# Optimization experiments

Hardware: AMD Instinct MI355X
Metric: run time of the kernel (lower is better)

The kernel has to match this reference:

```python
import jax, jax.numpy as jnp
import numpy as np

N, C, H, W = 32, 1, 512, 1024
SAMPLE_NUM = 5000
SIGMA = 0.03
ALPHA = 1.0
EPS = 1e-6
LOSS_WEIGHT = 1.0


def setup_inputs() -> dict:
    key = jax.random.key(0)
    k0, k1, k2, k3 = jax.random.split(key, 4)
    prediction = jax.random.normal(k0, (N, C, H, W), dtype=jnp.float32)
    # depths strictly > 0 so target > mask_value (=-1e-8) holds for every pixel,
    # matching the common case where all pixels are 'effective'.
    target = jax.random.uniform(k1, (N, C, H, W), dtype=jnp.float32,
                                minval=0.1, maxval=10.0)
    mask = jax.random.randint(k2, (N, C, H, W), 0, 2).astype(bool)
    # per-image random permutation of pixel indices -> disjoint pairs (A, B),
    # reproducing torch.randperm-based pair sampling as constant indices.
    perm = jax.vmap(lambda k: jax.random.permutation(k, H * W))(
        jax.random.split(k3, N))                      # [N, H*W] int32
    idx_A = perm[:, 0:2 * SAMPLE_NUM:2]               # [N, S]
    idx_B = perm[:, 1:2 * SAMPLE_NUM:2]               # [N, S]
    return {"prediction": prediction, "target": target, "mask": mask,
            "idx_A": idx_A, "idx_B": idx_B}


def reference(prediction, target, mask, idx_A, idx_B):
    n = target.shape[0]
    p = prediction.reshape(n, -1)   # [N, H*W]
    t = target.reshape(n, -1)
    m = mask.reshape(n, -1)

    iA = jnp.take_along_axis(p, idx_A, axis=1)   # [N, S]
    iB = jnp.take_along_axis(p, idx_B, axis=1)
    tA = jnp.take_along_axis(t, idx_A, axis=1)
    tB = jnp.take_along_axis(t, idx_B, axis=1)
    mA = jnp.take_along_axis(m, idx_A, axis=1)
    mB = jnpp_take(m, idx_B) if False else jnp.take_along_axis(m, idx_B, axis=1)

    ratio = tA / (tB + EPS)
    hi = 1.0 + SIGMA
    lo = 1.0 / (1.0 + SIGMA)
    mask_eq = (ratio < hi) & (ratio > lo)
    labels = jnp.where(ratio >= hi, 1.0,
                       jnp.where(ratio <= lo, -1.0, 0.0)).astype(p.dtype)
    cmask = mA & mB

    eq_sel = mask_eq & cmask
    uneq_sel = (~mask_eq) & cmask

    equal_loss = jnp.where(eq_sel, (iA - iB) ** 2, 0.0).sum()
    unequal_loss = jnp.where(
        uneq_sel, jnp.log1p(jnp.exp((iB - iA) * labels)), 0.0).sum()
    valid_samples = cmask.sum().astype(p.dtype)

    loss = (ALPHA * equal_loss + unequal_loss) / (valid_samples + EPS)
    return loss * LOSS_WEIGHT
```

## Files before the change

kernel.cpp:

```cpp
#include <hip/hip_runtime.h>
#include <math.h>

#define SAMPLE_NUM 5000
#define HWSZ (512 * 1024)
#define SIGMA_F 0.03f
#define EPS_F 1e-6f

template <bool MASK_I32>
__device__ __forceinline__ void
process_pairs(const float* __restrict__ pred, const float* __restrict__ targ,
              const void* __restrict__ mask_raw, const int* __restrict__ idxA,
              const int* __restrict__ idxB, int total, float& eq_sum,
              float& uneq_sum, float& valid) {
  const float hi = 1.0f + SIGMA_F;
  const float lo = 1.0f / (1.0f + SIGMA_F);
  const int* m32 = (const int*)mask_raw;
  const unsigned char* m8 = (const unsigned char*)mask_raw;

  const int i = blockIdx.x * blockDim.x + threadIdx.x;
  if (i >= total) return;

  const int n = i / SAMPLE_NUM;
  const long long base = (long long)n * HWSZ;
  const int a = idxA[i];
  const int b = idxB[i];
  const long long ia_off = base + a;
  const long long ib_off = base + b;

  const int ma = MASK_I32 ? m32[ia_off] : (int)m8[ia_off];
  const int mb = MASK_I32 ? m32[ib_off] : (int)m8[ib_off];
  const float tA = targ[ia_off];
  const float tB = targ[ib_off];
  const float iA = pred[ia_off];
  const float iB = pred[ib_off];

  const bool cm = (ma != 0) && (mb != 0);
  const float ratio = tA / (tB + EPS_F);
  const bool is_eq = (ratio < hi) && (ratio > lo);
  const float d = iA - iB;
  const float label = (ratio >= hi) ? 1.0f : -1.0f;
  const float x = (iB - iA) * label;
  const float u = (x > 20.0f) ? x : log1pf(expf(x));

  eq_sum += (cm && is_eq) ? d * d : 0.0f;
  uneq_sum += (cm && !is_eq) ? u : 0.0f;
  valid += cm ? 1.0f : 0.0f;
}

__global__ void __launch_bounds__(256)
ranking_loss_kernel(const float* __restrict__ pred,
                    const float* __restrict__ targ,
                    const void* __restrict__ mask_raw,
                    const int* __restrict__ idxA,
                    const int* __restrict__ idxB,
                    float* __restrict__ out,
                    float* __restrict__ ws,
                    int total) {
  const unsigned int* mw = (const unsigned int*)mask_raw;
  bool mask_is_i32 = true;
  #pragma unroll
  for (int w = 0; w < 32; ++w) {
    if (mw[w] > 1u) mask_is_i32 = false;
  }

  float eq_sum = 0.0f, uneq_sum = 0.0f, valid = 0.0f;
  if (mask_is_i32) {
    process_pairs<true>(pred, targ, mask_raw, idxA, idxB, total, eq_sum,
                        uneq_sum, valid);
  } else {
    process_pairs<false>(pred, targ, mask_raw, idxA, idxB, total, eq_sum,
                         uneq_sum, valid);
  }

  #pragma unroll
  for (int off = 32; off > 0; off >>= 1) {
    eq_sum   += __shfl_down(eq_sum, off, 64);
    uneq_sum += __shfl_down(uneq_sum, off, 64);
    valid    += __shfl_down(valid, off, 64);
  }

  __shared__ float s_eq[4], s_un[4], s_va[4];
  const int lane = threadIdx.x & 63;
  const int wave = threadIdx.x >> 6;
  if (lane == 0) {
    s_eq[wave] = eq_sum;
    s_un[wave] = uneq_sum;
    s_va[wave] = valid;
  }
  __syncthreads();

  if (threadIdx.x == 0) {
    float e = 0.0f, u = 0.0f, v = 0.0f;
    const int nwaves = blockDim.x >> 6;
    for (int w = 0; w < nwaves; ++w) {
      e += s_eq[w];
      u += s_un[w];
      v += s_va[w];
    }
    atomicAdd(&ws[0], e);
    atomicAdd(&ws[1], u);
    atomicAdd(&ws[2], v);
    __threadfence();
    const unsigned int ticket = atomicAdd((unsigned int*)&ws[3], 1u);
    if (ticket == gridDim.x - 1) {
      const float eqs = atomicAdd(&ws[0], 0.0f);
      const float uns = atomicAdd(&ws[1], 0.0f);
      const float vas = atomicAdd(&ws[2], 0.0f);
      out[0] = (eqs + uns) / (vas + EPS_F);
    }
  }
}

extern "C" void kernel_launch(void* const* d_in, const int* in_sizes, int n_in,
                              void* d_out, int out_size, void* d_ws,
                              size_t ws_size, hipStream_t stream) {
  const float* pred = (const float*)d_in[0];
  const float* targ = (const float*)d_in[1];
  const void* mask = d_in[2];
  const int* idxA = (const int*)d_in[3];
  const int* idxB = (const int*)d_in[4];
  float* out = (float*)d_out;
  float* ws = (float*)d_ws;

  const int total = in_sizes[3];

  hipMemsetAsync(d_ws, 0, 4 * sizeof(float), stream);

  const int block = 256;
  const int grid = (total + block - 1) / block;
  ranking_loss_kernel<<<grid, block, 0, stream>>>(pred, targ, mask, idxA, idxB,
                                                  out, ws, total);
}
```

Measured before the change: 208.3 us.

## Replace atomic ticket reduction with per-block partials and finalize kernel; skip masked loads

Each block now writes its three partial sums to its own workspace slot, and a second single-block kernel reduces those slots and computes the loss. This removes the memset and the contended global float atomics and ticket counter, at the cost of one extra kernel launch. The per-pair body also loads target and prediction only when both mask bits are set, which skips gather traffic for masked pairs but adds divergent branches.

```diff
diff --git a/kernel.cpp b/kernel.cpp
--- a/kernel.cpp
+++ b/kernel.cpp
@@ -5,19 +5,21 @@
 #define HWSZ (512 * 1024)
 #define SIGMA_F 0.03f
 #define EPS_F 1e-6f
+#define BLOCK 256
+
 
 template <bool MASK_I32>
 __device__ __forceinline__ void
-process_pairs(const float* __restrict__ pred, const float* __restrict__ targ,
-              const void* __restrict__ mask_raw, const int* __restrict__ idxA,
-              const int* __restrict__ idxB, int total, float& eq_sum,
-              float& uneq_sum, float& valid) {
+pair_body(const float* __restrict__ pred, const float* __restrict__ targ,
+          const void* __restrict__ mask_raw, const int* __restrict__ idxA,
+          const int* __restrict__ idxB, int total, float& eq_sum,
+          float& uneq_sum, float& valid) {
   const float hi = 1.0f + SIGMA_F;
   const float lo = 1.0f / (1.0f + SIGMA_F);
   const int* m32 = (const int*)mask_raw;
   const unsigned char* m8 = (const unsigned char*)mask_raw;
 
-  const int i = blockIdx.x * blockDim.x + threadIdx.x;
+  const int i = blockIdx.x * BLOCK + threadIdx.x;
   if (i >= total) return;
 
   const int n = i / SAMPLE_NUM;
@@ -29,33 +31,33 @@
 
   const int ma = MASK_I32 ? m32[ia_off] : (int)m8[ia_off];
   const int mb = MASK_I32 ? m32[ib_off] : (int)m8[ib_off];
-  const float tA = targ[ia_off];
-  const float tB = targ[ib_off];
-  const float iA = pred[ia_off];
-  const float iB = pred[ib_off];
 
-  const bool cm = (ma != 0) && (mb != 0);
-  const float ratio = tA / (tB + EPS_F);
-  const bool is_eq = (ratio < hi) && (ratio > lo);
-  const float d = iA - iB;
-  const float label = (ratio >= hi) ? 1.0f : -1.0f;
-  const float x = (iB - iA) * label;
-  const float u = (x > 20.0f) ? x : log1pf(expf(x));
+  if (ma && mb) {
+    const float tA = targ[ia_off];
+    const float tB = targ[ib_off];
+    const float iA = pred[ia_off];
+    const float iB = pred[ib_off];
 
-  eq_sum += (cm && is_eq) ? d * d : 0.0f;
-  uneq_sum += (cm && !is_eq) ? u : 0.0f;
-  valid += cm ? 1.0f : 0.0f;
+    valid += 1.0f;
+    const float ratio = tA / (tB + EPS_F);
+    if (ratio < hi && ratio > lo) {
+      const float d = iA - iB;
+      eq_sum += d * d;
+    } else {
+      const float label = (ratio >= hi) ? 1.0f : -1.0f;
+      const float x = (iB - iA) * label;
+      uneq_sum += (x > 20.0f) ? x : log1pf(expf(x));
+    }
+  }
 }
 
-__global__ void __launch_bounds__(256)
-ranking_loss_kernel(const float* __restrict__ pred,
-                    const float* __restrict__ targ,
-                    const void* __restrict__ mask_raw,
-                    const int* __restrict__ idxA,
-                    const int* __restrict__ idxB,
-                    float* __restrict__ out,
-                    float* __restrict__ ws,
-                    int total) {
+__global__ void __launch_bounds__(BLOCK)
+ranking_loss_partial(const float* __restrict__ pred,
+                     const float* __restrict__ targ,
+                     const void* __restrict__ mask_raw,
+                     const int* __restrict__ idxA,
+                     const int* __restrict__ idxB,
+                     float* __restrict__ ws, int total) {
   const unsigned int* mw = (const unsigned int*)mask_raw;
   bool mask_is_i32 = true;
   #pragma unroll
@@ -65,11 +67,11 @@
 
   float eq_sum = 0.0f, uneq_sum = 0.0f, valid = 0.0f;
   if (mask_is_i32) {
-    process_pairs<true>(pred, targ, mask_raw, idxA, idxB, total, eq_sum,
-                        uneq_sum, valid);
+    pair_body<true>(pred, targ, mask_raw, idxA, idxB, total, eq_sum, uneq_sum,
+                    valid);
   } else {
-    process_pairs<false>(pred, targ, mask_raw, idxA, idxB, total, eq_sum,
-                         uneq_sum, valid);
+    pair_body<false>(pred, targ, mask_raw, idxA, idxB, total, eq_sum, uneq_sum,
+                     valid);
   }
 
   #pragma unroll
@@ -91,23 +93,52 @@
 
   if (threadIdx.x == 0) {
     float e = 0.0f, u = 0.0f, v = 0.0f;
-    const int nwaves = blockDim.x >> 6;
-    for (int w = 0; w < nwaves; ++w) {
+    #pragma unroll
+    for (int w = 0; w < BLOCK / 64; ++w) {
       e += s_eq[w];
       u += s_un[w];
       v += s_va[w];
     }
-    atomicAdd(&ws[0], e);
-    atomicAdd(&ws[1], u);
-    atomicAdd(&ws[2], v);
-    __threadfence();
-    const unsigned int ticket = atomicAdd((unsigned int*)&ws[3], 1u);
-    if (ticket == gridDim.x - 1) {
-      const float eqs = atomicAdd(&ws[0], 0.0f);
-      const float uns = atomicAdd(&ws[1], 0.0f);
-      const float vas = atomicAdd(&ws[2], 0.0f);
-      out[0] = (eqs + uns) / (vas + EPS_F);
+    float* slot = ws + 3 * blockIdx.x;
+    slot[0] = e;
+    slot[1] = u;
+    slot[2] = v;
+  }
+}
+
+__global__ void __launch_bounds__(BLOCK)
+ranking_loss_finalize(const float* __restrict__ ws, float* __restrict__ out,
+                      int nblocks) {
+  float e = 0.0f, u = 0.0f, v = 0.0f;
+  for (int s = threadIdx.x; s < nblocks; s += BLOCK) {
+    e += ws[3 * s + 0];
+    u += ws[3 * s + 1];
+    v += ws[3 * s + 2];
+  }
+  #pragma unroll
+  for (int off = 32; off > 0; off >>= 1) {
+    e += __shfl_down(e, off, 64);
+    u += __shfl_down(u, off, 64);
+    v += __shfl_down(v, off, 64);
+  }
+  __shared__ float s_e[4], s_u[4], s_v[4];
+  const int lane = threadIdx.x & 63;
+  const int wave = threadIdx.x >> 6;
+  if (lane == 0) {
+    s_e[wave] = e;
+    s_u[wave] = u;
+    s_v[wave] = v;
+  }
+  __syncthreads();
+  if (threadIdx.x == 0) {
+    float te = 0.0f, tu = 0.0f, tv = 0.0f;
+    #pragma unroll
+    for (int w = 0; w < BLOCK / 64; ++w) {
+      te += s_e[w];
+      tu += s_u[w];
+      tv += s_v[w];
     }
+    out[0] = (te + tu) / (tv + EPS_F);
   }
 }
 
@@ -123,11 +154,9 @@
   float* ws = (float*)d_ws;
 
   const int total = in_sizes[3];
+  const int grid = (total + BLOCK - 1) / BLOCK;
 
-  hipMemsetAsync(d_ws, 0, 4 * sizeof(float), stream);
-
-  const int block = 256;
-  const int grid = (total + block - 1) / block;
-  ranking_loss_kernel<<<grid, block, 0, stream>>>(pred, targ, mask, idxA, idxB,
-                                                  out, ws, total);
+  ranking_loss_partial<<<grid, BLOCK, 0, stream>>>(pred, targ, mask, idxA,
+                                                   idxB, ws, total);
+  ranking_loss_finalize<<<1, BLOCK, 0, stream>>>(ws, out, grid);
 }
```

After: 170.6 us. 1.22x faster.
